# Kernel optimization log

Hardware: AMD Instinct MI355X
Metric: run time of the kernel (lower is better)

Reference implementation:

```python
import jax, jax.numpy as jnp
import numpy as np

N_HEAD = 16
N_EMBD = 1024

def setup_inputs() -> dict:
    key = jax.random.key(0)
    ks = jax.random.split(key, 9)
    B, T, C = 4, 2048, N_EMBD
    s = 1.0 / np.sqrt(C)
    return {
        "x": jax.random.normal(ks[0], (B, T, C), dtype=jnp.float32),
        "Wk": jax.random.normal(ks[1], (C, C), dtype=jnp.float32) * s,
        "bk": jnp.zeros((C,), dtype=jnp.float32),
        "Wq": jax.random.normal(ks[2], (C, C), dtype=jnp.float32) * s,
        "bq": jnp.zeros((C,), dtype=jnp.float32),
        "Wv": jax.random.normal(ks[3], (C, C), dtype=jnp.float32) * s,
        "bv": jnp.zeros((C,), dtype=jnp.float32),
        "Wp": jax.random.normal(ks[4], (C, C), dtype=jnp.float32) * s,
        "bp": jnp.zeros((C,), dtype=jnp.float32),
    }

def reference(x, Wk, bk, Wq, bq, Wv, bv, Wp, bp):
    B, T, C = x.shape
    H = N_HEAD
    D = C // H  # head dim
    # linear projections (torch nn.Linear: x @ W^T + b)
    def proj(W, b):
        y = jnp.einsum('btc,oc->bto', x, W) + b
        return y.reshape(B, T, H, D).transpose(0, 2, 1, 3)  # b h t d
    k = proj(Wk, bk)
    q = proj(Wq, bq)
    v = proj(Wv, bv)
    scale = 1.0 / jnp.sqrt(jnp.float32(D))
    att = jnp.einsum('bhtd,bhsd->bhts', q, k) * scale  # [B,H,T,T]
    mask = jnp.tril(jnp.ones((T, T), dtype=bool))
    att = jnp.where(mask[None, None], att, -jnp.inf)
    att = jax.nn.softmax(att, axis=-1)
    y = jnp.einsum('bhts,bhsd->bhtd', att, v)
    y = y.transpose(0, 2, 1, 3).reshape(B, T, C)
    y = jnp.einsum('btc,oc->bto', y, Wp) + bp
    return y
```

## Files before the change

### kernel.cpp

```cpp
#include <hip/hip_runtime.h>
#include <hip/hip_bf16.h>
#include <stdint.h>

#define NH 16
#define CD 1024
#define DD 64
#define TT 2048
#define BB 4
#define MR (BB*TT)

typedef float f32x4 __attribute__((ext_vector_type(4)));
typedef short s16x8 __attribute__((ext_vector_type(8)));

static __device__ __forceinline__ uint16_t f2bf(float f) {
  uint32_t u = __float_as_uint(f);
  u += 0x7FFFu + ((u >> 16) & 1u);
  return (uint16_t)(u >> 16);
}

__global__ __launch_bounds__(256)
void cvt5(const float* __restrict__ x, const float* __restrict__ wq,
          const float* __restrict__ wk, const float* __restrict__ wv,
          const float* __restrict__ wp,
          uint16_t* __restrict__ xb, uint16_t* __restrict__ wqb,
          uint16_t* __restrict__ wkb, uint16_t* __restrict__ wvb,
          uint16_t* __restrict__ wpb)
{
  const int XN8 = (MR*CD)/8;
  const int WN8 = (CD*CD)/8;
  int i = blockIdx.x*256 + threadIdx.x;
  const float* src; uint16_t* dst; int off;
  if (i < XN8) { src = x; dst = xb; off = i; }
  else {
    int r = i - XN8; int ws = r / WN8; off = r - ws*WN8;
    src = (ws==0)?wq:(ws==1)?wk:(ws==2)?wv:wp;
    dst = (ws==0)?wqb:(ws==1)?wkb:(ws==2)?wvb:wpb;
  }
  f32x4 a = *(const f32x4*)&src[(size_t)off*8];
  f32x4 b = *(const f32x4*)&src[(size_t)off*8 + 4];
  s16x8 o;
  o[0]=(short)f2bf(a.x); o[1]=(short)f2bf(a.y); o[2]=(short)f2bf(a.z); o[3]=(short)f2bf(a.w);
  o[4]=(short)f2bf(b.x); o[5]=(short)f2bf(b.y); o[6]=(short)f2bf(b.z); o[7]=(short)f2bf(b.w);
  *(s16x8*)&dst[(size_t)off*8] = o;
}

#define GQ_SBAR  { __builtin_amdgcn_s_barrier(); __builtin_amdgcn_sched_barrier(0); }
#define GQ_LGKM  { asm volatile("s_waitcnt lgkmcnt(0)" ::: "memory"); __builtin_amdgcn_sched_barrier(0); }
#define GQ_VM3   { asm volatile("s_waitcnt vmcnt(3)" ::: "memory"); __builtin_amdgcn_sched_barrier(0); }
#define GQ_VM0   { asm volatile("s_waitcnt vmcnt(0)" ::: "memory"); __builtin_amdgcn_sched_barrier(0); }

#define GQ_PHASE(DB, KH, STG, VM) { \
  GQ_SBAR \
  s16x8 af[4], bf[4]; \
  _Pragma("unroll") \
  for (int i = 0; i < 4; ++i) { \
    int row = wr*64 + i*16 + r16; \
    af[i] = *(const s16x8*)&lA[DB][KH][row*32 + sw8]; \
  } \
  _Pragma("unroll") \
  for (int j = 0; j < 4; ++j) { \
    int row = wc*64 + j*16 + r16; \
    bf[j] = *(const s16x8*)&lB[DB][KH][row*32 + sw8]; \
  } \
  STG; \
  GQ_LGKM \
  __builtin_amdgcn_s_setprio(1); \
  if (!vt) { \
    _Pragma("unroll") \
    for (int i = 0; i < 4; ++i) \
      _Pragma("unroll") \
      for (int j = 0; j < 4; ++j) \
        acc[i][j] = __builtin_amdgcn_mfma_f32_16x16x32_bf16(af[i], bf[j], acc[i][j], 0,0,0); \
  } else { \
    _Pragma("unroll") \
    for (int i = 0; i < 4; ++i) \
      _Pragma("unroll") \
      for (int j = 0; j < 4; ++j) \
        acc[i][j] = __builtin_amdgcn_mfma_f32_16x16x32_bf16(bf[j], af[i], acc[i][j], 0,0,0); \
  } \
  __builtin_amdgcn_s_setprio(0); \
  VM \
}

__global__ __launch_bounds__(512)
void gemm_qkv8(const uint16_t* __restrict__ xb, const uint16_t* __restrict__ wqkv,
               const float* __restrict__ bq, const float* __restrict__ bk,
               const float* __restrict__ bv,
               uint16_t* __restrict__ qo, uint16_t* __restrict__ ko,
               uint16_t* __restrict__ vo)
{
  __shared__ __align__(16) uint16_t lA[2][2][128*32];
  __shared__ __align__(16) uint16_t lB[2][2][256*32];

  const int tid = threadIdx.x, lane = tid & 63;
  const int g = lane >> 4, r16 = lane & 15;
  const int w = tid >> 6;
  const int wr = w >> 2, wc = w & 3;
  const int sw8 = ((g ^ ((r16 >> 1) & 3)) << 3);

  const int bid = blockIdx.x;
  const int lin = (bid & 7)*96 + (bid >> 3);
  const int cx = lin >> 6, my = lin & 63;
  const int rowBase = my * 128, colBase = cx * 256;
  const int z = colBase >> 10;
  const bool vt = (z == 2);
  const float* bias  = (z==0) ? bq : (z==1) ? bk : bv;
  uint16_t* Out      = (z==0) ? qo : (z==1) ? ko : vo;
  const float oscale = (z==0) ? 0.125f : 1.0f;

  auto stageA = [&](int dbuf, int kh, int kt) {
    const int row = w*16 + (lane >> 2);
    const int k = kt*64 + kh*32 + (((lane & 3) ^ ((row >> 1) & 3)) << 3);
    __builtin_amdgcn_global_load_lds(
      (const void*)(xb + (size_t)(rowBase + row)*CD + k),
      (void*)&lA[dbuf][kh][(w*16)*32], 16, 0, 0);
  };
  auto stageB = [&](int dbuf, int kh, int kt) {
    #pragma unroll
    for (int c = 0; c < 2; ++c) {
      const int r0 = (c*8 + w)*16;
      const int row = r0 + (lane >> 2);
      const int k = kt*64 + kh*32 + (((lane & 3) ^ ((row >> 1) & 3)) << 3);
      __builtin_amdgcn_global_load_lds(
        (const void*)(wqkv + (size_t)(colBase + row)*CD + k),
        (void*)&lB[dbuf][kh][r0*32], 16, 0, 0);
    }
  };

  f32x4 acc[4][4];
  #pragma unroll
  for (int i = 0; i < 4; ++i)
    #pragma unroll
    for (int j = 0; j < 4; ++j) acc[i][j] = (f32x4){0.f,0.f,0.f,0.f};

  stageA(0, 0, 0); stageB(0, 0, 0);
  stageA(0, 1, 0); stageB(0, 1, 0);
  GQ_VM3

  for (int t = 0; t < 8; ++t) {
    const int kt1 = 2*t + 1, kt2 = 2*t + 2;
    const bool last = (t == 7);
    GQ_PHASE(0, 0, { stageA(1,0,kt1); stageB(1,0,kt1); }, GQ_VM3)
    GQ_PHASE(0, 1, { stageA(1,1,kt1); stageB(1,1,kt1); }, GQ_VM3)
    GQ_PHASE(1, 0, if (!last) { stageA(0,0,kt2); stageB(0,0,kt2); },
                   if (!last) GQ_VM3 else GQ_VM0)
    GQ_PHASE(1, 1, if (!last) { stageA(0,1,kt2); stageB(0,1,kt2); },
                   if (!last) GQ_VM3)
  }

  if (!vt) {
    #pragma unroll
    for (int i = 0; i < 4; ++i)
      #pragma unroll
      for (int j = 0; j < 4; ++j) {
        int n = colBase + wc*64 + j*16 + r16;
        int nl = n & 1023;
        float bb = bias[nl];
        int hh = nl >> 6, d = nl & (DD-1);
        #pragma unroll
        for (int rg = 0; rg < 4; ++rg) {
          int m = rowBase + wr*64 + i*16 + g*4 + rg;
          int b = m >> 11, t = m & (TT-1);
          Out[(((size_t)(b*NH + hh))*TT + t)*DD + d] = f2bf((acc[i][j][rg] + bb) * oscale);
        }
      }
  } else {
    #pragma unroll
    for (int i = 0; i < 4; ++i)
      #pragma unroll
      for (int j = 0; j < 4; ++j) {
        int m = rowBase + wr*64 + i*16 + r16;
        int b = m >> 11, t = m & (TT-1);
        #pragma unroll
        for (int rg = 0; rg < 4; ++rg) {
          int n = colBase + wc*64 + j*16 + g*4 + rg;
          int nl = n & 1023;
          float bb = bias[nl];
          int hh = nl >> 6, d = nl & (DD-1);
          Out[(((size_t)(b*NH + hh))*DD + d)*TT + t] = f2bf(acc[i][j][rg] + bb);
        }
      }
  }
}

__global__ __launch_bounds__(512)
void gemm_proj8(const uint16_t* __restrict__ yb, const uint16_t* __restrict__ wpb,
                const float* __restrict__ bias, float* __restrict__ Out)
{
  __shared__ __align__(16) uint16_t lA[2][2][128*32];
  __shared__ __align__(16) uint16_t lB[2][2][256*32];

  const int tid = threadIdx.x, lane = tid & 63;
  const int g = lane >> 4, r16 = lane & 15;
  const int w = tid >> 6;
  const int wr = w >> 2, wc = w & 3;
  const int sw8 = ((g ^ ((r16 >> 1) & 3)) << 3);
  const bool vt = false;

  const int bid = blockIdx.x;
  const int lin = (bid & 7)*32 + (bid >> 3);
  const int cx = lin >> 6, my = lin & 63;
  const int rowBase = my * 128, colBase = cx * 256;

  auto stageA = [&](int dbuf, int kh, int kt) {
    const int row = w*16 + (lane >> 2);
    const int k = kt*64 + kh*32 + (((lane & 3) ^ ((row >> 1) & 3)) << 3);
    __builtin_amdgcn_global_load_lds(
      (const void*)(yb + (size_t)(rowBase + row)*CD + k),
      (void*)&lA[dbuf][kh][(w*16)*32], 16, 0, 0);
  };
  auto stageB = [&](int dbuf, int kh, int kt) {
    #pragma unroll
    for (int c = 0; c < 2; ++c) {
      const int r0 = (c*8 + w)*16;
      const int row = r0 + (lane >> 2);
      const int k = kt*64 + kh*32 + (((lane & 3) ^ ((row >> 1) & 3)) << 3);
      __builtin_amdgcn_global_load_lds(
        (const void*)(wpb + (size_t)(colBase + row)*CD + k),
        (void*)&lB[dbuf][kh][r0*32], 16, 0, 0);
    }
  };

  f32x4 acc[4][4];
  #pragma unroll
  for (int i = 0; i < 4; ++i)
    #pragma unroll
    for (int j = 0; j < 4; ++j) acc[i][j] = (f32x4){0.f,0.f,0.f,0.f};

  stageA(0, 0, 0); stageB(0, 0, 0);
  stageA(0, 1, 0); stageB(0, 1, 0);
  GQ_VM3

  for (int t = 0; t < 8; ++t) {
    const int kt1 = 2*t + 1, kt2 = 2*t + 2;
    const bool last = (t == 7);
    GQ_PHASE(0, 0, { stageA(1,0,kt1); stageB(1,0,kt1); }, GQ_VM3)
    GQ_PHASE(0, 1, { stageA(1,1,kt1); stageB(1,1,kt1); }, GQ_VM3)
    GQ_PHASE(1, 0, if (!last) { stageA(0,0,kt2); stageB(0,0,kt2); },
                   if (!last) GQ_VM3 else GQ_VM0)
    GQ_PHASE(1, 1, if (!last) { stageA(0,1,kt2); stageB(0,1,kt2); },
                   if (!last) GQ_VM3)
  }

  #pragma unroll
  for (int i = 0; i < 4; ++i)
    #pragma unroll
    for (int j = 0; j < 4; ++j) {
      int n = colBase + wc*64 + j*16 + r16;
      float bb = bias[n];
      #pragma unroll
      for (int rg = 0; rg < 4; ++rg) {
        int m = rowBase + wr*64 + i*16 + g*4 + rg;
        Out[(size_t)m*CD + n] = acc[i][j][rg] + bb;
      }
    }
}

__global__ __launch_bounds__(256)
void attn128s(const uint16_t* __restrict__ qg, const uint16_t* __restrict__ kg,
              const uint16_t* __restrict__ vtg, uint16_t* __restrict__ yg)
{
  __shared__ __align__(16) uint16_t lK[2][64*64];
  __shared__ __align__(16) uint16_t lV[2][64*64];
  __shared__ __align__(16) uint16_t lP[4][16*64];

  const int tid = threadIdx.x, lane = tid & 63;
  const int g = lane >> 4, r16 = lane & 15;
  const int w = tid >> 6;
  const int id  = blockIdx.x;
  const int xcd = id & 7, idx = id >> 3;
  const int gid = xcd + 8*(idx >> 3);
  const int xq  = idx & 7;
  const int h = gid & 15, b = gid >> 4;
  const size_t kbase = ((size_t)(b*NH + h)) * TT * DD;
  const size_t vbase = ((size_t)(b*NH + h)) * DD * TT;

  const short oe = (r16 == 0) ? (short)0x3F80 : (short)0;
  const s16x8 onesf = {oe,oe,oe,oe,oe,oe,oe,oe};

  auto stage = [&](int cur, int jt) {
    #pragma unroll
    for (int c = 0; c < 2; ++c) {
      int row = w*16 + c*8 + (lane >> 3);
      int sc  = (lane & 7) ^ (row & 7);
      __builtin_amdgcn_global_load_lds(
        (const void*)(kg + kbase + (size_t)(jt*64 + row)*DD + sc*8),
        (void*)&lK[cur][(w*16 + c*8)*64], 16, 0, 0);
      __builtin_amdgcn_global_load_lds(
        (const void*)(vtg + vbase + (size_t)row*TT + jt*64 + sc*8),
        (void*)&lV[cur][(w*16 + c*8)*64], 16, 0, 0);
    }
  };

  for (int ph = 0; ph < 2; ++ph) {
    const int qbi = ph ? 15 - xq : xq;
    const int qrow0 = qbi*128 + w*32;

    s16x8 qf[2][2];
    #pragma unroll
    for (int rb = 0; rb < 2; ++rb)
      #pragma unroll
      for (int ks = 0; ks < 2; ++ks)
        qf[rb][ks] = *(const s16x8*)&qg[kbase + (size_t)(qrow0 + rb*16 + r16)*DD + ks*32 + g*8];

    f32x4 accY[2][4];
    f32x4 accL[2];
    #pragma unroll
    for (int rb = 0; rb < 2; ++rb) {
      #pragma unroll
      for (int i = 0; i < 4; ++i) accY[rb][i] = (f32x4){0.f,0.f,0.f,0.f};
      accL[rb] = (f32x4){0.f,0.f,0.f,0.f};
    }

    const int njt = 2*qbi + 2;
    __syncthreads();
    stage(0, 0);
    int cur = 0;
    for (int jt = 0; jt < njt; ++jt) {
      __syncthreads();
      if (jt + 1 < njt) stage(cur ^ 1, jt + 1);
      if (jt*64 <= qrow0 + 31) {
        f32x4 sacc[2][4];
        #pragma unroll
        for (int rb = 0; rb < 2; ++rb)
          #pragma unroll
          for (int sb = 0; sb < 4; ++sb) sacc[rb][sb] = (f32x4){0.f,0.f,0.f,0.f};
        __builtin_amdgcn_s_setprio(1);
        #pragma unroll
        for (int sb = 0; sb < 4; ++sb)
          #pragma unroll
          for (int ks = 0; ks < 2; ++ks) {
            int row = sb*16 + r16;
            int ch = (ks*4 + g) ^ (row & 7);
            s16x8 kf = *(const s16x8*)&lK[cur][row*64 + ch*8];
            sacc[0][sb] = __builtin_amdgcn_mfma_f32_16x16x32_bf16(qf[0][ks], kf, sacc[0][sb], 0,0,0);
            sacc[1][sb] = __builtin_amdgcn_mfma_f32_16x16x32_bf16(qf[1][ks], kf, sacc[1][sb], 0,0,0);
          }
        __builtin_amdgcn_s_setprio(0);
        s16x8 vfr[2][4];
        #pragma unroll
        for (int ks = 0; ks < 2; ++ks)
          #pragma unroll
          for (int dblk = 0; dblk < 4; ++dblk) {
            int row = dblk*16 + r16;
            int ch = (ks*4 + g) ^ (row & 7);
            vfr[ks][dblk] = *(const s16x8*)&lV[cur][row*64 + ch*8];
          }
        #pragma unroll
        for (int rb = 0; rb < 2; ++rb) {
          const int qr0b = qrow0 + rb*16;
          if (jt*64 > qr0b + 15) continue;
          if (jt*64 + 63 > qr0b) {
            #pragma unroll
            for (int sb = 0; sb < 4; ++sb)
              #pragma unroll
              for (int rg = 0; rg < 4; ++rg)
                if (jt*64 + sb*16 + r16 > qr0b + g*4 + rg) sacc[rb][sb][rg] = -1.0e30f;
          }
          #pragma unroll
          for (int sb = 0; sb < 4; ++sb) {
            int c = sb*16 + r16;
            #pragma unroll
            for (int rgp = 0; rgp < 2; ++rgp) {
              float2 fp;
              fp.x = __expf(sacc[rb][sb][2*rgp]);
              fp.y = __expf(sacc[rb][sb][2*rgp + 1]);
              __hip_bfloat162 h2 = __float22bfloat162_rn(fp);
              uint32_t u = *(uint32_t*)&h2;
              int row0 = g*4 + 2*rgp;
              lP[w][row0*64 + (((c>>3) ^ (row0&7))<<3) + (c&7)] = (uint16_t)(u & 0xffffu);
              int row1 = row0 + 1;
              lP[w][row1*64 + (((c>>3) ^ (row1&7))<<3) + (c&7)] = (uint16_t)(u >> 16);
            }
          }
          s16x8 pf[2];
          #pragma unroll
          for (int ks = 0; ks < 2; ++ks)
            pf[ks] = *(const s16x8*)&lP[w][r16*64 + (((ks*4 + g) ^ (r16&7))<<3)];
          __builtin_amdgcn_s_setprio(1);
          #pragma unroll
          for (int ks = 0; ks < 2; ++ks) {
            #pragma unroll
            for (int dblk = 0; dblk < 4; ++dblk)
              accY[rb][dblk] = __builtin_amdgcn_mfma_f32_16x16x32_bf16(pf[ks], vfr[ks][dblk], accY[rb][dblk], 0,0,0);
            accL[rb] = __builtin_amdgcn_mfma_f32_16x16x32_bf16(pf[ks], onesf, accL[rb], 0,0,0);
          }
          __builtin_amdgcn_s_setprio(0);
        }
      }
      cur ^= 1;
    }

    #pragma unroll
    for (int rb = 0; rb < 2; ++rb) {
      float ls[4];
      #pragma unroll
      for (int rg = 0; rg < 4; ++rg)
        ls[rg] = __shfl(accL[rb][rg], lane & 48);
      #pragma unroll
      for (int dblk = 0; dblk < 4; ++dblk) {
        int d = dblk*16 + r16;
        #pragma unroll
        for (int rg = 0; rg < 4; ++rg) {
          int t = qrow0 + rb*16 + g*4 + rg;
          yg[((size_t)b*TT + t)*CD + h*DD + d] = f2bf(accY[rb][dblk][rg] / ls[rg]);
        }
      }
    }
  }
}

template<int OM>
__global__ __launch_bounds__(256)
void gemm128o(const void* __restrict__ Aptr, const float* __restrict__ W,
              const float* __restrict__ bias, void* __restrict__ Out, float oscale)
{
  __shared__ __align__(16) uint16_t lA[128*40];
  __shared__ __align__(16) uint16_t lB[128*40];
  const int tid = threadIdx.x, lane = tid & 63;
  const int g = lane >> 4, r16 = lane & 15;
  const int w = tid >> 6, wr = w >> 1, wc = w & 1;
  const int rowBase = blockIdx.y * 128, colBase = blockIdx.x * 128;

  f32x4 acc[4][4];
  #pragma unroll
  for (int i = 0; i < 4; ++i)
    #pragma unroll
    for (int j = 0; j < 4; ++j) acc[i][j] = (f32x4){0.f,0.f,0.f,0.f};

  for (int k0 = 0; k0 < CD; k0 += 32) {
    if (OM != 1) {
      const float* A = (const float*)Aptr;
      #pragma unroll
      for (int p = 0; p < 4; ++p) {
        int rr = p*32 + (tid >> 3), kc = (tid & 7)*4;
        f32x4 v = *(const f32x4*)&A[(size_t)(rowBase + rr)*CD + k0 + kc];
        uint64_t pk = (uint64_t)f2bf(v.x) | ((uint64_t)f2bf(v.y)<<16)
                    | ((uint64_t)f2bf(v.z)<<32) | ((uint64_t)f2bf(v.w)<<48);
        *(uint64_t*)&lA[rr*40 + kc] = pk;
      }
    } else {
      const uint16_t* A = (const uint16_t*)Aptr;
      #pragma unroll
      for (int p = 0; p < 2; ++p) {
        int rr = p*64 + (tid >> 2), kc = (tid & 3)*8;
        *(s16x8*)&lA[rr*40 + kc] = *(const s16x8*)&A[(size_t)(rowBase + rr)*CD + k0 + kc];
      }
    }
    #pragma unroll
    for (int p = 0; p < 4; ++p) {
      int rr = p*32 + (tid >> 3), kc = (tid & 7)*4;
      f32x4 v = *(const f32x4*)&W[(size_t)(colBase + rr)*CD + k0 + kc];
      uint64_t pk = (uint64_t)f2bf(v.x) | ((uint64_t)f2bf(v.y)<<16)
                  | ((uint64_t)f2bf(v.z)<<32) | ((uint64_t)f2bf(v.w)<<48);
      *(uint64_t*)&lB[rr*40 + kc] = pk;
    }
    __syncthreads();
    s16x8 af[4], bfr[4];
    #pragma unroll
    for (int i = 0; i < 4; ++i) {
      af[i]  = *(const s16x8*)&lA[(wr*64 + i*16 + r16)*40 + g*8];
      bfr[i] = *(const s16x8*)&lB[(wc*64 + i*16 + r16)*40 + g*8];
    }
    if (OM != 2) {
      #pragma unroll
      for (int i = 0; i < 4; ++i)
        #pragma unroll
        for (int j = 0; j < 4; ++j)
          acc[i][j] = __builtin_amdgcn_mfma_f32_16x16x32_bf16(af[i], bfr[j], acc[i][j], 0,0,0);
    } else {
      #pragma unroll
      for (int i = 0; i < 4; ++i)
        #pragma unroll
        for (int j = 0; j < 4; ++j)
          acc[i][j] = __builtin_amdgcn_mfma_f32_16x16x32_bf16(bfr[j], af[i], acc[i][j], 0,0,0);
    }
    __syncthreads();
  }

  #pragma unroll
  for (int i = 0; i < 4; ++i)
    #pragma unroll
    for (int j = 0; j < 4; ++j) {
      if (OM == 0) {
        int n = colBase + wc*64 + j*16 + r16;
        float bb = bias[n];
        int hh = n >> 6, d = n & (DD-1);
        #pragma unroll
        for (int rg = 0; rg < 4; ++rg) {
          int m = rowBase + wr*64 + i*16 + g*4 + rg;
          int b = m >> 11, t = m & (TT-1);
          ((uint16_t*)Out)[(((size_t)(b*NH + hh))*TT + t)*DD + d] = f2bf((acc[i][j][rg] + bb) * oscale);
        }
      } else if (OM == 1) {
        int n = colBase + wc*64 + j*16 + r16;
        float bb = bias[n];
        #pragma unroll
        for (int rg = 0; rg < 4; ++rg) {
          int m = rowBase + wr*64 + i*16 + g*4 + rg;
          ((float*)Out)[(size_t)m*CD + n] = acc[i][j][rg] + bb;
        }
      } else {
        int m = rowBase + wr*64 + i*16 + r16;
        int b = m >> 11, t = m & (TT-1);
        #pragma unroll
        for (int rg = 0; rg < 4; ++rg) {
          int n = colBase + wc*64 + j*16 + g*4 + rg;
          float bb = bias[n];
          int hh = n >> 6, d = n & (DD-1);
          ((uint16_t*)Out)[(((size_t)(b*NH + hh))*DD + d)*TT + t] = f2bf(acc[i][j][rg] + bb);
        }
      }
    }
}

extern "C" void kernel_launch(void* const* d_in, const int* in_sizes, int n_in,
                              void* d_out, int out_size, void* d_ws, size_t ws_size,
                              hipStream_t stream)
{
  const float* x  = (const float*)d_in[0];
  const float* Wk = (const float*)d_in[1];
  const float* bk = (const float*)d_in[2];
  const float* Wq = (const float*)d_in[3];
  const float* bq = (const float*)d_in[4];
  const float* Wv = (const float*)d_in[5];
  const float* bv = (const float*)d_in[6];
  const float* Wp = (const float*)d_in[7];
  const float* bp = (const float*)d_in[8];
  float* out = (float*)d_out;

  const size_t elems = (size_t)MR * CD;
  const size_t welems = (size_t)CD * CD;

  if (ws_size >= 76ull*1024*1024) {
    uint16_t* xbf = (uint16_t*)d_ws;
    uint16_t* wqb = xbf + elems;
    uint16_t* wkb = wqb + welems;
    uint16_t* wvb = wkb + welems;
    uint16_t* wpb = wvb + welems;
    uint16_t* q_ws = wpb + welems;
    uint16_t* k_ws = q_ws + elems;
    uint16_t* v_ws = k_ws + elems;
    uint16_t* y_ws = xbf;

    cvt5<<<6144, 256, 0, stream>>>(x, Wq, Wk, Wv, Wp, xbf, wqb, wkb, wvb, wpb);
    gemm_qkv8<<<768, 512, 0, stream>>>(xbf, wqb, bq, bk, bv, q_ws, k_ws, v_ws);
    attn128s<<<512, 256, 0, stream>>>(q_ws, k_ws, v_ws, y_ws);
    gemm_proj8<<<256, 512, 0, stream>>>(y_ws, wpb, bp, out);
  } else {
    uint16_t* q_ws = (uint16_t*)d_ws;
    uint16_t* k_ws = q_ws + elems;
    uint16_t* v_ws = k_ws + elems;
    uint16_t* y_ws = v_ws + elems;
    dim3 gg(CD/128, MR/128);
    gemm128o<0><<<gg, 256, 0, stream>>>(x, Wq, bq, q_ws, 0.125f);
    gemm128o<0><<<gg, 256, 0, stream>>>(x, Wk, bk, k_ws, 1.0f);
    gemm128o<2><<<gg, 256, 0, stream>>>(x, Wv, bv, v_ws, 1.0f);
    attn128s<<<512, 256, 0, stream>>>(q_ws, k_ws, v_ws, y_ws);
    gemm128o<1><<<gg, 256, 0, stream>>>(y_ws, Wp, bp, out, 1.0f);
  }
}
```

Baseline: 189.5 us.

## Triple-buffer QKV GEMM LDS pipeline with prefetch two k-tiles ahead

Replaces the double-buffered QKV projection GEMM with a triple-buffered version that stages whole 64-wide k-tiles two iterations ahead and keeps up to six async global-to-LDS loads in flight. Each iteration now does one barrier and 32 MFMAs instead of two half-tile phases of 16 each. The aim is to hide global load latency better and cut barrier count. The cost is LDS use rising from 96KB to 144KB per block and larger fragment register pressure, which could limit occupancy.

```diff
diff --git a/kernel.cpp b/kernel.cpp
--- a/kernel.cpp
+++ b/kernel.cpp
@@ -47,9 +47,148 @@
 #define GQ_SBAR  { __builtin_amdgcn_s_barrier(); __builtin_amdgcn_sched_barrier(0); }
 #define GQ_LGKM  { asm volatile("s_waitcnt lgkmcnt(0)" ::: "memory"); __builtin_amdgcn_sched_barrier(0); }
 #define GQ_VM3   { asm volatile("s_waitcnt vmcnt(3)" ::: "memory"); __builtin_amdgcn_sched_barrier(0); }
+#define GQ_VM6   { asm volatile("s_waitcnt vmcnt(6)" ::: "memory"); __builtin_amdgcn_sched_barrier(0); }
 #define GQ_VM0   { asm volatile("s_waitcnt vmcnt(0)" ::: "memory"); __builtin_amdgcn_sched_barrier(0); }
 
-#define GQ_PHASE(DB, KH, STG, VM) { \
+__global__ __launch_bounds__(512)
+void gemm_qkv8m(const uint16_t* __restrict__ xb, const uint16_t* __restrict__ wqkv,
+                const float* __restrict__ bq, const float* __restrict__ bk,
+                const float* __restrict__ bv,
+                uint16_t* __restrict__ qo, uint16_t* __restrict__ ko,
+                uint16_t* __restrict__ vo)
+{
+  __shared__ __align__(16) uint16_t lA[3][2][128*32];
+  __shared__ __align__(16) uint16_t lB[3][2][256*32];
+
+  const int tid = threadIdx.x, lane = tid & 63;
+  const int g = lane >> 4, r16 = lane & 15;
+  const int w = tid >> 6;
+  const int wr = w >> 2, wc = w & 3;
+  const int sw8 = ((g ^ ((r16 >> 1) & 3)) << 3);
+
+  const int bid = blockIdx.x;
+  const int lin = (bid & 7)*96 + (bid >> 3);
+  const int cx = lin >> 6, my = lin & 63;
+  const int rowBase = my * 128, colBase = cx * 256;
+  const int z = colBase >> 10;
+  const bool vt = (z == 2);
+  const float* bias  = (z==0) ? bq : (z==1) ? bk : bv;
+  uint16_t* Out      = (z==0) ? qo : (z==1) ? ko : vo;
+  const float oscale = (z==0) ? 0.125f : 1.0f;
+
+  auto stageA = [&](int buf, int kh, int kt) {
+    const int row = w*16 + (lane >> 2);
+    const int k = kt*64 + kh*32 + (((lane & 3) ^ ((row >> 1) & 3)) << 3);
+    __builtin_amdgcn_global_load_lds(
+      (const void*)(xb + (size_t)(rowBase + row)*CD + k),
+      (void*)&lA[buf][kh][(w*16)*32], 16, 0, 0);
+  };
+  auto stageB = [&](int buf, int kh, int kt) {
+    #pragma unroll
+    for (int c = 0; c < 2; ++c) {
+      const int r0 = (c*8 + w)*16;
+      const int row = r0 + (lane >> 2);
+      const int k = kt*64 + kh*32 + (((lane & 3) ^ ((row >> 1) & 3)) << 3);
+      __builtin_amdgcn_global_load_lds(
+        (const void*)(wqkv + (size_t)(colBase + row)*CD + k),
+        (void*)&lB[buf][kh][r0*32], 16, 0, 0);
+    }
+  };
+  auto stageTile = [&](int buf, int kt) {
+    stageA(buf, 0, kt); stageB(buf, 0, kt);
+    stageA(buf, 1, kt); stageB(buf, 1, kt);
+  };
+
+  f32x4 acc[4][4];
+  #pragma unroll
+  for (int i = 0; i < 4; ++i)
+    #pragma unroll
+    for (int j = 0; j < 4; ++j) acc[i][j] = (f32x4){0.f,0.f,0.f,0.f};
+
+  stageTile(0, 0);
+  stageTile(1, 1);
+  GQ_VM6
+
+  int cur = 0;
+  for (int t = 0; t < 16; ++t) {
+    const int nxt2 = (cur + 2 >= 3) ? cur - 1 : cur + 2;
+    GQ_SBAR
+    s16x8 af[2][4], bf[2][4];
+    #pragma unroll
+    for (int kh = 0; kh < 2; ++kh) {
+      #pragma unroll
+      for (int i = 0; i < 4; ++i) {
+        int row = wr*64 + i*16 + r16;
+        af[kh][i] = *(const s16x8*)&lA[cur][kh][row*32 + sw8];
+      }
+      #pragma unroll
+      for (int j = 0; j < 4; ++j) {
+        int row = wc*64 + j*16 + r16;
+        bf[kh][j] = *(const s16x8*)&lB[cur][kh][row*32 + sw8];
+      }
+    }
+    if (t < 14) stageTile(nxt2, t + 2);
+    GQ_LGKM
+    __builtin_amdgcn_s_setprio(1);
+    if (!vt) {
+      #pragma unroll
+      for (int kh = 0; kh < 2; ++kh)
+        #pragma unroll
+        for (int i = 0; i < 4; ++i)
+          #pragma unroll
+          for (int j = 0; j < 4; ++j)
+            acc[i][j] = __builtin_amdgcn_mfma_f32_16x16x32_bf16(af[kh][i], bf[kh][j], acc[i][j], 0,0,0);
+    } else {
+      #pragma unroll
+      for (int kh = 0; kh < 2; ++kh)
+        #pragma unroll
+        for (int i = 0; i < 4; ++i)
+          #pragma unroll
+          for (int j = 0; j < 4; ++j)
+            acc[i][j] = __builtin_amdgcn_mfma_f32_16x16x32_bf16(bf[kh][j], af[kh][i], acc[i][j], 0,0,0);
+    }
+    __builtin_amdgcn_s_setprio(0);
+    if (t < 14)      GQ_VM6
+    else if (t == 14) GQ_VM0
+    cur = (cur == 2) ? 0 : cur + 1;
+  }
+
+  if (!vt) {
+    #pragma unroll
+    for (int i = 0; i < 4; ++i)
+      #pragma unroll
+      for (int j = 0; j < 4; ++j) {
+        int n = colBase + wc*64 + j*16 + r16;
+        int nl = n & 1023;
+        float bb = bias[nl];
+        int hh = nl >> 6, d = nl & (DD-1);
+        #pragma unroll
+        for (int rg = 0; rg < 4; ++rg) {
+          int m = rowBase + wr*64 + i*16 + g*4 + rg;
+          int b = m >> 11, t2 = m & (TT-1);
+          Out[(((size_t)(b*NH + hh))*TT + t2)*DD + d] = f2bf((acc[i][j][rg] + bb) * oscale);
+        }
+      }
+  } else {
+    #pragma unroll
+    for (int i = 0; i < 4; ++i)
+      #pragma unroll
+      for (int j = 0; j < 4; ++j) {
+        int m = rowBase + wr*64 + i*16 + r16;
+        int b = m >> 11, t2 = m & (TT-1);
+        #pragma unroll
+        for (int rg = 0; rg < 4; ++rg) {
+          int n = colBase + wc*64 + j*16 + g*4 + rg;
+          int nl = n & 1023;
+          float bb = bias[nl];
+          int hh = nl >> 6, d = nl & (DD-1);
+          Out[(((size_t)(b*NH + hh))*DD + d)*TT + t2] = f2bf(acc[i][j][rg] + bb);
+        }
+      }
+  }
+}
+
+#define GP_PHASE(DB, KH, STG, VM) { \
   GQ_SBAR \
   s16x8 af[4], bf[4]; \
   _Pragma("unroll") \
@@ -65,122 +204,13 @@
   STG; \
   GQ_LGKM \
   __builtin_amdgcn_s_setprio(1); \
-  if (!vt) { \
+  _Pragma("unroll") \
+  for (int i = 0; i < 4; ++i) \
     _Pragma("unroll") \
-    for (int i = 0; i < 4; ++i) \
-      _Pragma("unroll") \
-      for (int j = 0; j < 4; ++j) \
-        acc[i][j] = __builtin_amdgcn_mfma_f32_16x16x32_bf16(af[i], bf[j], acc[i][j], 0,0,0); \
-  } else { \
-    _Pragma("unroll") \
-    for (int i = 0; i < 4; ++i) \
-      _Pragma("unroll") \
-      for (int j = 0; j < 4; ++j) \
-        acc[i][j] = __builtin_amdgcn_mfma_f32_16x16x32_bf16(bf[j], af[i], acc[i][j], 0,0,0); \
-  } \
+    for (int j = 0; j < 4; ++j) \
+      acc[i][j] = __builtin_amdgcn_mfma_f32_16x16x32_bf16(af[i], bf[j], acc[i][j], 0,0,0); \
   __builtin_amdgcn_s_setprio(0); \
   VM \
-}
-
-__global__ __launch_bounds__(512)
-void gemm_qkv8(const uint16_t* __restrict__ xb, const uint16_t* __restrict__ wqkv,
-               const float* __restrict__ bq, const float* __restrict__ bk,
-               const float* __restrict__ bv,
-               uint16_t* __restrict__ qo, uint16_t* __restrict__ ko,
-               uint16_t* __restrict__ vo)
-{
-  __shared__ __align__(16) uint16_t lA[2][2][128*32];
-  __shared__ __align__(16) uint16_t lB[2][2][256*32];
-
-  const int tid = threadIdx.x, lane = tid & 63;
-  const int g = lane >> 4, r16 = lane & 15;
-  const int w = tid >> 6;
-  const int wr = w >> 2, wc = w & 3;
-  const int sw8 = ((g ^ ((r16 >> 1) & 3)) << 3);
-
-  const int bid = blockIdx.x;
-  const int lin = (bid & 7)*96 + (bid >> 3);
-  const int cx = lin >> 6, my = lin & 63;
-  const int rowBase = my * 128, colBase = cx * 256;
-  const int z = colBase >> 10;
-  const bool vt = (z == 2);
-  const float* bias  = (z==0) ? bq : (z==1) ? bk : bv;
-  uint16_t* Out      = (z==0) ? qo : (z==1) ? ko : vo;
-  const float oscale = (z==0) ? 0.125f : 1.0f;
-
-  auto stageA = [&](int dbuf, int kh, int kt) {
-    const int row = w*16 + (lane >> 2);
-    const int k = kt*64 + kh*32 + (((lane & 3) ^ ((row >> 1) & 3)) << 3);
-    __builtin_amdgcn_global_load_lds(
-      (const void*)(xb + (size_t)(rowBase + row)*CD + k),
-      (void*)&lA[dbuf][kh][(w*16)*32], 16, 0, 0);
-  };
-  auto stageB = [&](int dbuf, int kh, int kt) {
-    #pragma unroll
-    for (int c = 0; c < 2; ++c) {
-      const int r0 = (c*8 + w)*16;
-      const int row = r0 + (lane >> 2);
-      const int k = kt*64 + kh*32 + (((lane & 3) ^ ((row >> 1) & 3)) << 3);
-      __builtin_amdgcn_global_load_lds(
-        (const void*)(wqkv + (size_t)(colBase + row)*CD + k),
-        (void*)&lB[dbuf][kh][r0*32], 16, 0, 0);
-    }
-  };
-
-  f32x4 acc[4][4];
-  #pragma unroll
-  for (int i = 0; i < 4; ++i)
-    #pragma unroll
-    for (int j = 0; j < 4; ++j) acc[i][j] = (f32x4){0.f,0.f,0.f,0.f};
-
-  stageA(0, 0, 0); stageB(0, 0, 0);
-  stageA(0, 1, 0); stageB(0, 1, 0);
-  GQ_VM3
-
-  for (int t = 0; t < 8; ++t) {
-    const int kt1 = 2*t + 1, kt2 = 2*t + 2;
-    const bool last = (t == 7);
-    GQ_PHASE(0, 0, { stageA(1,0,kt1); stageB(1,0,kt1); }, GQ_VM3)
-    GQ_PHASE(0, 1, { stageA(1,1,kt1); stageB(1,1,kt1); }, GQ_VM3)
-    GQ_PHASE(1, 0, if (!last) { stageA(0,0,kt2); stageB(0,0,kt2); },
-                   if (!last) GQ_VM3 else GQ_VM0)
-    GQ_PHASE(1, 1, if (!last) { stageA(0,1,kt2); stageB(0,1,kt2); },
-                   if (!last) GQ_VM3)
-  }
-
-  if (!vt) {
-    #pragma unroll
-    for (int i = 0; i < 4; ++i)
-      #pragma unroll
-      for (int j = 0; j < 4; ++j) {
-        int n = colBase + wc*64 + j*16 + r16;
-        int nl = n & 1023;
-        float bb = bias[nl];
-        int hh = nl >> 6, d = nl & (DD-1);
-        #pragma unroll
-        for (int rg = 0; rg < 4; ++rg) {
-          int m = rowBase + wr*64 + i*16 + g*4 + rg;
-          int b = m >> 11, t = m & (TT-1);
-          Out[(((size_t)(b*NH + hh))*TT + t)*DD + d] = f2bf((acc[i][j][rg] + bb) * oscale);
-        }
-      }
-  } else {
-    #pragma unroll
-    for (int i = 0; i < 4; ++i)
-      #pragma unroll
-      for (int j = 0; j < 4; ++j) {
-        int m = rowBase + wr*64 + i*16 + r16;
-        int b = m >> 11, t = m & (TT-1);
-        #pragma unroll
-        for (int rg = 0; rg < 4; ++rg) {
-          int n = colBase + wc*64 + j*16 + g*4 + rg;
-          int nl = n & 1023;
-          float bb = bias[nl];
-          int hh = nl >> 6, d = nl & (DD-1);
-          Out[(((size_t)(b*NH + hh))*DD + d)*TT + t] = f2bf(acc[i][j][rg] + bb);
-        }
-      }
-  }
 }
 
 __global__ __launch_bounds__(512)
@@ -195,7 +225,6 @@
   const int w = tid >> 6;
   const int wr = w >> 2, wc = w & 3;
   const int sw8 = ((g ^ ((r16 >> 1) & 3)) << 3);
-  const bool vt = false;
 
   const int bid = blockIdx.x;
   const int lin = (bid & 7)*32 + (bid >> 3);
@@ -234,11 +263,11 @@
   for (int t = 0; t < 8; ++t) {
     const int kt1 = 2*t + 1, kt2 = 2*t + 2;
     const bool last = (t == 7);
-    GQ_PHASE(0, 0, { stageA(1,0,kt1); stageB(1,0,kt1); }, GQ_VM3)
-    GQ_PHASE(0, 1, { stageA(1,1,kt1); stageB(1,1,kt1); }, GQ_VM3)
-    GQ_PHASE(1, 0, if (!last) { stageA(0,0,kt2); stageB(0,0,kt2); },
+    GP_PHASE(0, 0, { stageA(1,0,kt1); stageB(1,0,kt1); }, GQ_VM3)
+    GP_PHASE(0, 1, { stageA(1,1,kt1); stageB(1,1,kt1); }, GQ_VM3)
+    GP_PHASE(1, 0, if (!last) { stageA(0,0,kt2); stageB(0,0,kt2); },
                    if (!last) GQ_VM3 else GQ_VM0)
-    GQ_PHASE(1, 1, if (!last) { stageA(0,1,kt2); stageB(0,1,kt2); },
+    GP_PHASE(1, 1, if (!last) { stageA(0,1,kt2); stageB(0,1,kt2); },
                    if (!last) GQ_VM3)
   }
 
@@ -544,7 +573,7 @@
     uint16_t* y_ws = xbf;
 
     cvt5<<<6144, 256, 0, stream>>>(x, Wq, Wk, Wv, Wp, xbf, wqb, wkb, wvb, wpb);
-    gemm_qkv8<<<768, 512, 0, stream>>>(xbf, wqb, bq, bk, bv, q_ws, k_ws, v_ws);
+    gemm_qkv8m<<<768, 512, 0, stream>>>(xbf, wqb, bq, bk, bv, q_ws, k_ws, v_ws);
     attn128s<<<512, 256, 0, stream>>>(q_ws, k_ws, v_ws, y_ws);
     gemm_proj8<<<256, 512, 0, stream>>>(y_ws, wpb, bp, out);
   } else {
```

Measured after the change: 180.2 us. -4.9%, faster.
